# Performance work log

Hardware: AMD Instinct MI355X
Metric: run time of the kernel (lower is better)

The kernel has to match this reference:

```python
import jax, jax.numpy as jnp
import numpy as np

DIM = 32
N_HOP = 2
N_MEMORY = 32
BATCH = 2048
N_ENTITY = 100000
N_RELATION = 48


def _gru_cell(x, h, w_ih, w_hh, b_ih, b_hh):
    # PyTorch GRUCell semantics
    gi = x @ w_ih.T + b_ih          # [b, 3d]
    gh = h @ w_hh.T + b_hh          # [b, 3d]
    i_r, i_z, i_n = jnp.split(gi, 3, axis=-1)
    h_r, h_z, h_n = jnp.split(gh, 3, axis=-1)
    r = jax.nn.sigmoid(i_r + h_r)
    z = jax.nn.sigmoid(i_z + h_z)
    n = jnp.tanh(i_n + r * h_n)
    return (1.0 - z) * n + z * h


def setup_inputs() -> dict:
    key = jax.random.key(0)
    ks = jax.random.split(key, 16)
    h_i = jax.random.randint(ks[0], (BATCH, N_HOP, N_MEMORY), 0, N_ENTITY)
    R_i = jax.random.randint(ks[1], (BATCH, N_HOP, N_MEMORY), 0, N_RELATION)
    t_i = jax.random.randint(ks[2], (BATCH, N_HOP, N_MEMORY), 0, N_ENTITY)
    v_i = jax.random.randint(ks[3], (BATCH,), 0, N_ENTITY)
    s = 0.05
    entity_emb = jax.random.normal(ks[4], (N_ENTITY, DIM), jnp.float32) * s
    relation_emb = jax.random.normal(ks[5], (N_RELATION, DIM, DIM), jnp.float32) * s
    agg_w1 = jax.random.normal(ks[6], (DIM, 4 * DIM), jnp.float32) * s
    agg_b1 = jnp.zeros((DIM,), jnp.float32)
    agg_w2 = jax.random.normal(ks[7], (1, DIM), jnp.float32) * s
    agg_b2 = jnp.zeros((1,), jnp.float32)
    gru_w_ih = jax.random.normal(ks[8], (N_HOP, 3 * DIM, DIM), jnp.float32) * s
    gru_w_hh = jax.random.normal(ks[9], (N_HOP, 3 * DIM, DIM), jnp.float32) * s
    gru_b_ih = jnp.zeros((N_HOP, 3 * DIM), jnp.float32)
    gru_b_hh = jnp.zeros((N_HOP, 3 * DIM), jnp.float32)
    ans_w = jax.random.normal(ks[10], (DIM, DIM), jnp.float32) * s
    ans_b = jnp.zeros((DIM,), jnp.float32)
    return {
        'h_i': h_i, 'R_i': R_i, 't_i': t_i, 'v_i': v_i,
        'entity_emb': entity_emb, 'relation_emb': relation_emb,
        'agg_w1': agg_w1, 'agg_b1': agg_b1, 'agg_w2': agg_w2, 'agg_b2': agg_b2,
        'gru_w_ih': gru_w_ih, 'gru_w_hh': gru_w_hh,
        'gru_b_ih': gru_b_ih, 'gru_b_hh': gru_b_hh,
        'ans_w': ans_w, 'ans_b': ans_b,
    }


def reference(h_i, R_i, t_i, v_i, entity_emb, relation_emb,
              agg_w1, agg_b1, agg_w2, agg_b2,
              gru_w_ih, gru_w_hh, gru_b_ih, gru_b_hh,
              ans_w, ans_b):
    # InputModule: embedding gathers
    vs = entity_emb[v_i]                     # [b, d]
    hs = entity_emb[h_i]                     # [b, H, m, d]
    ts = entity_emb[t_i]                     # [b, H, m, d]
    Rs = relation_emb[R_i]                   # [b, H, m, d, d]

    M = vs
    n_hop = hs.shape[1]
    for hop in range(n_hop):
        R = Rs[:, hop]                       # [b, m, d, d]
        h = hs[:, hop]                       # [b, m, d]
        t = ts[:, hop]                       # [b, m, d]
        Rh = jnp.einsum('bmij,bmj->bmi', R, h)   # [b, m, d]
        vexp = vs[:, None, :]
        mexp = M[:, None, :]
        z = jnp.concatenate([Rh * vexp, Rh * mexp,
                             jnp.abs(Rh - vexp), jnp.abs(Rh - mexp)], axis=2)  # [b, m, 4d]
        # AggregateFnc: tanh(Linear) -> Linear(d,1); dropout is eval-mode identity
        Z = jnp.tanh(z @ agg_w1.T + agg_b1) @ agg_w2.T + agg_b2   # [b, m, 1]
        g = jax.nn.softmax(Z[..., 0], axis=1)[..., None]           # [b, m, 1]
        o = jnp.sum(t * g, axis=1)                                 # [b, d]
        M = _gru_cell(o, M, gru_w_ih[hop], gru_w_hh[hop],
                      gru_b_ih[hop], gru_b_hh[hop])
    # AnswerModule (dropout = identity in eval)
    Mw = jax.nn.sigmoid(M @ ans_w.T + ans_b)
    return jnp.sum(vs * Mw, axis=1)          # [b]
```

## Files before the change

kernel.cpp:

```cpp
#include <hip/hip_runtime.h>
#include <hip/hip_bf16.h>


#define NHOP 2

typedef __attribute__((ext_vector_type(4)))  float f32x4;
typedef __attribute__((ext_vector_type(8)))  short bf16x8s;
typedef __attribute__((ext_vector_type(4)))  int   i32x4;

__device__ __forceinline__ float sigmoid_f(float x){ return 1.0f/(1.0f+__expf(-x)); }
__device__ __forceinline__ float tanh_f(float x){
  float e = __expf(2.0f*x);
  return 1.0f - 2.0f/(e + 1.0f);
}
__device__ __forceinline__ unsigned pk_bf16(float lo, float hi){
  __hip_bfloat162 h = __float22bfloat162_rn(make_float2(lo, hi));
  return *reinterpret_cast<unsigned*>(&h);
}

__global__ __launch_bounds__(256) void ripple_fused(
    const int* __restrict__ h_i, const int* __restrict__ R_i, const int* __restrict__ t_i,
    const int* __restrict__ v_i,
    const float* __restrict__ entity_emb, const float* __restrict__ relation_emb,
    const float* __restrict__ agg_w1, const float* __restrict__ agg_b1,
    const float* __restrict__ agg_w2, const float* __restrict__ agg_b2,
    const float* __restrict__ gru_w_ih, const float* __restrict__ gru_w_hh,
    const float* __restrict__ gru_b_ih, const float* __restrict__ gru_b_hh,
    const float* __restrict__ ans_w, const float* __restrict__ ans_b,
    float* __restrict__ out)
{
  __shared__ __align__(16) int   s_bfrag[8*64*4];
  __shared__ __align__(16) float s_rhA[2][32*33];
  __shared__ __align__(16) float s_vsM[32*2];
  __shared__ __align__(16) float s_zpart[64];
  __shared__ __align__(16) float s_opart[8*32];
  __shared__ __align__(16) float s_M  [32];
  __shared__ __align__(16) float s_gig[192];

  const int b   = blockIdx.x;
  const int tid = threadIdx.x;
  const int g   = tid >> 5;
  const int o   = tid & 31;
  const int l   = tid & 63;
  const int w   = tid >> 6;
  const int c   = o & 7;
  const int r_  = o >> 3;
  const bool bb4 = (c & 4) != 0;
  const bool bb2 = (c & 2) != 0;
  const bool bb1 = (c & 1) != 0;

  #pragma unroll
  for (int k = 0; k < 2; ++k){
    int s  = tid + k*256;
    int f  = s >> 6, li = s & 63;
    int x  = f >> 1, ot = f & 1;
    const float* src = agg_w1 + (ot*16 + (li & 15))*128 + x*32 + ((li >> 4) & 3)*8;
    float4 f0 = *(const float4*)src;
    float4 f1 = *(const float4*)(src + 4);
    *(int4*)&s_bfrag[s*4] = make_int4((int)pk_bf16(f0.x, f0.y), (int)pk_bf16(f0.z, f0.w),
                                      (int)pk_bf16(f1.x, f1.y), (int)pk_bf16(f1.z, f1.w));
  }
  float Mreg = 0.f;
  if (tid < 32){
    float v = entity_emb[(size_t)v_i[b]*32 + o];
    s_vsM[o*2+0] = v; s_vsM[o*2+1] = v; s_M[o] = v;
    Mreg = v;
  }

  {
    const int iA = c*4 + r_;
    #pragma unroll 1
    for (int it = 0; it < 2*4; ++it){
      const int hp = it >> 2;
      const int ml = it & 3;
      const int ibase = (b*NHOP + hp)*32;
      int m    = g*4 + ml;
      int ridx = R_i[ibase + m];
      int hidx = h_i[ibase + m];
      const float* Rbase = relation_emb + (size_t)ridx*1024;
      float4 hv = *(const float4*)(entity_emb + (size_t)hidx*32 + c*4);
      float p[8];
      #pragma unroll
      for (int q = 0; q < 8; ++q){
        float4 rv = *(const float4*)(Rbase + q*128 + o*4);
        p[q] = rv.x*hv.x + rv.y*hv.y + rv.z*hv.z + rv.w*hv.w;
      }
      #pragma unroll
      for (int k = 0; k < 4; ++k){
        float send = bb4 ? p[k] : p[k+4];
        float t = __shfl_xor(send, 4);
        p[k] = (bb4 ? p[k+4] : p[k]) + t;
      }
      #pragma unroll
      for (int k = 0; k < 2; ++k){
        float send = bb2 ? p[k] : p[k+2];
        float t = __shfl_xor(send, 2);
        p[k] = (bb2 ? p[k+2] : p[k]) + t;
      }
      {
        float send = bb1 ? p[0] : p[1];
        float t = __shfl_xor(send, 1);
        p[0] = (bb1 ? p[1] : p[0]) + t;
      }
      s_rhA[hp][m*33 + iA] = p[0];
    }
  }
  __syncthreads();

  const int mt  = w >> 1, ot = w & 1;
  const int col = l & 15;
  const int kg  = l >> 4;
  const float b1o = agg_b1[ot*16 + col];
  const float w2o = agg_w2[ot*16 + col];

  for (int hop = 0; hop < NHOP; ++hop){
    const int ibase = (b*NHOP + hop)*32;

    float tv[4];
    #pragma unroll
    for (int ml = 0; ml < 4; ++ml)
      tv[ml] = entity_emb[(size_t)t_i[ibase + g*4 + ml]*32 + o];

    {
      const int m = mt*16 + col;
      const float* rp = &s_rhA[hop][m*33 + kg*8];
      float4 q0 = *(const float4*)(rp);
      float4 q1 = *(const float4*)(rp + 4);
      float rh[8] = {q0.x,q0.y,q0.z,q0.w,q1.x,q1.y,q1.z,q1.w};
      unsigned aw[4][4];
      #pragma unroll
      for (int q = 0; q < 4; ++q){
        int i0 = kg*8 + 2*q;
        float2 vm0 = *(const float2*)&s_vsM[i0*2];
        float2 vm1 = *(const float2*)&s_vsM[(i0+1)*2];
        float e0 = rh[2*q], e1 = rh[2*q+1];
        aw[0][q] = pk_bf16(e0*vm0.x,        e1*vm1.x);
        aw[1][q] = pk_bf16(e0*vm0.y,        e1*vm1.y);
        aw[2][q] = pk_bf16(fabsf(e0-vm0.x), fabsf(e1-vm1.x));
        aw[3][q] = pk_bf16(fabsf(e0-vm0.y), fabsf(e1-vm1.y));
      }
      f32x4 acc = {0.f, 0.f, 0.f, 0.f};
      #pragma unroll
      for (int x = 0; x < 4; ++x){
        i32x4 av = {(int)aw[x][0], (int)aw[x][1], (int)aw[x][2], (int)aw[x][3]};
        i32x4 bv = *(const i32x4*)&s_bfrag[((x*2 + ot)*64 + l)*4];
        acc = __builtin_amdgcn_mfma_f32_16x16x32_bf16(
                __builtin_bit_cast(bf16x8s, av),
                __builtin_bit_cast(bf16x8s, bv), acc, 0, 0, 0);
      }
      float v[4];
      #pragma unroll
      for (int r = 0; r < 4; ++r) v[r] = tanh_f(acc[r] + b1o) * w2o;
      const bool b3 = (l & 8) != 0;
      #pragma unroll
      for (int k = 0; k < 2; ++k){
        float send = b3 ? v[k] : v[k+2];
        float tt = __shfl_xor(send, 8);
        v[k] = (b3 ? v[k+2] : v[k]) + tt;
      }
      const bool b2_ = (l & 4) != 0;
      {
        float send = b2_ ? v[0] : v[1];
        float tt = __shfl_xor(send, 4);
        v[0] = (b2_ ? v[1] : v[0]) + tt;
      }
      v[0] += __shfl_xor(v[0], 2);
      v[0] += __shfl_xor(v[0], 1);
      if ((l & 3) == 0){
        int m_local = kg*4 + ((l >> 3) & 1)*2 + ((l >> 2) & 1);
        s_zpart[ot*32 + mt*16 + m_local] = v[0];
      }
    }
    __syncthreads();

    {
      float z  = s_zpart[o] + s_zpart[32 + o];
      float mx = z;
      #pragma unroll
      for (int s = 16; s > 0; s >>= 1) mx = fmaxf(mx, __shfl_xor(mx, s));
      float e  = __expf(z - mx);
      float sm = e;
      #pragma unroll
      for (int s = 16; s > 0; s >>= 1) sm += __shfl_xor(sm, s);
      float gval = e / sm;
      float po = 0.f;
      #pragma unroll
      for (int ml = 0; ml < 4; ++ml)
        po += __shfl(gval, g*4 + ml) * tv[ml];
      s_opart[g*32 + o] = po;
    }
    __syncthreads();

    {
      const int cc = (tid & 7) * 4;
      const int rr = tid >> 3;
      float4 o4 = make_float4(0,0,0,0);
      #pragma unroll
      for (int gg = 0; gg < 8; ++gg){
        float4 t = *(const float4*)&s_opart[gg*32 + cc];
        o4.x += t.x; o4.y += t.y; o4.z += t.z; o4.w += t.w;
      }
      float4 m4 = *(const float4*)&s_M[cc];
      #pragma unroll
      for (int k = 0; k < 3; ++k){
        int row = k*32 + rr;
        float4 wi = *(const float4*)(gru_w_ih + ((size_t)hop*96 + row)*32 + cc);
        float4 wh = *(const float4*)(gru_w_hh + ((size_t)hop*96 + row)*32 + cc);
        float ai = wi.x*o4.x + wi.y*o4.y + wi.z*o4.z + wi.w*o4.w;
        float ah = wh.x*m4.x + wh.y*m4.y + wh.z*m4.z + wh.w*m4.w;
        ai += __shfl_xor(ai,1); ai += __shfl_xor(ai,2); ai += __shfl_xor(ai,4);
        ah += __shfl_xor(ah,1); ah += __shfl_xor(ah,2); ah += __shfl_xor(ah,4);
        if ((tid & 7) == 0){
          s_gig[row]      = ai;
          s_gig[96 + row] = ah;
        }
      }
    }
    __syncthreads();

    if (tid < 32){
      const float* bih = gru_b_ih + hop*96;
      const float* bhh = gru_b_hh + hop*96;
      float ir = s_gig[o]       + bih[o];
      float iz = s_gig[32 + o]  + bih[32 + o];
      float in_= s_gig[64 + o]  + bih[64 + o];
      float hr = s_gig[96 + o]  + bhh[o];
      float hz = s_gig[128 + o] + bhh[32 + o];
      float hn = s_gig[160 + o] + bhh[64 + o];
      float r  = sigmoid_f(ir + hr);
      float zz = sigmoid_f(iz + hz);
      float n  = tanh_f(in_ + r*hn);
      float Mn = (1.f - zz)*n + zz*Mreg;
      Mreg = Mn;
      s_M[o] = Mn;
      s_vsM[o*2+1] = Mn;
    }
    __syncthreads();
  }

  {
    const int cc = (tid & 7) * 4;
    const int rr = tid >> 3;
    float4 m4 = *(const float4*)&s_M[cc];
    float4 aw = *(const float4*)(ans_w + (size_t)rr*32 + cc);
    float a = aw.x*m4.x + aw.y*m4.y + aw.z*m4.z + aw.w*m4.w;
    a += __shfl_xor(a,1); a += __shfl_xor(a,2); a += __shfl_xor(a,4);
    if ((tid & 7) == 0) s_zpart[rr] = sigmoid_f(a + ans_b[rr]);
  }
  __syncthreads();
  if (tid < 32){
    float val = s_vsM[o*2+0] * s_zpart[o];
    #pragma unroll
    for (int s = 16; s > 0; s >>= 1) val += __shfl_xor(val, s);
    if (tid == 0) out[b] = val;
  }
}

extern "C" void kernel_launch(void* const* d_in, const int* in_sizes, int n_in,
                              void* d_out, int out_size, void* d_ws, size_t ws_size,
                              hipStream_t stream) {
  const int*   h_i          = (const int*)  d_in[0];
  const int*   R_i          = (const int*)  d_in[1];
  const int*   t_i          = (const int*)  d_in[2];
  const int*   v_i          = (const int*)  d_in[3];
  const float* entity_emb   = (const float*)d_in[4];
  const float* relation_emb = (const float*)d_in[5];
  const float* agg_w1       = (const float*)d_in[6];
  const float* agg_b1       = (const float*)d_in[7];
  const float* agg_w2       = (const float*)d_in[8];
  const float* agg_b2       = (const float*)d_in[9];
  const float* gru_w_ih     = (const float*)d_in[10];
  const float* gru_w_hh     = (const float*)d_in[11];
  const float* gru_b_ih     = (const float*)d_in[12];
  const float* gru_b_hh     = (const float*)d_in[13];
  const float* ans_w        = (const float*)d_in[14];
  const float* ans_b        = (const float*)d_in[15];
  (void)agg_b2;
  float* outp = (float*)d_out;

  const int batch = in_sizes[3];
  ripple_fused<<<batch, 256, 0, stream>>>(
      h_i, R_i, t_i, v_i, entity_emb, relation_emb,
      agg_w1, agg_b1, agg_w2, agg_b2,
      gru_w_ih, gru_w_hh, gru_b_ih, gru_b_hh,
      ans_w, ans_b, outp);
}
```

Before: 45.28 us.

## Process two batch elements per block to amortize setup and weight loads

```diff
diff --git a/kernel.cpp b/kernel.cpp
--- a/kernel.cpp
+++ b/kernel.cpp
@@ -16,6 +16,23 @@
 __device__ __forceinline__ unsigned pk_bf16(float lo, float hi){
   __hip_bfloat162 h = __float22bfloat162_rn(make_float2(lo, hi));
   return *reinterpret_cast<unsigned*>(&h);
+}
+__device__ __forceinline__ float bfly8(float p[8], bool bb4, bool bb2, bool bb1){
+  #pragma unroll
+  for (int k = 0; k < 4; ++k){
+    float send = bb4 ? p[k] : p[k+4];
+    float t = __shfl_xor(send, 4);
+    p[k] = (bb4 ? p[k+4] : p[k]) + t;
+  }
+  #pragma unroll
+  for (int k = 0; k < 2; ++k){
+    float send = bb2 ? p[k] : p[k+2];
+    float t = __shfl_xor(send, 2);
+    p[k] = (bb2 ? p[k+2] : p[k]) + t;
+  }
+  float send = bb1 ? p[0] : p[1];
+  float t = __shfl_xor(send, 1);
+  return (bb1 ? p[1] : p[0]) + t;
 }
 
 __global__ __launch_bounds__(256) void ripple_fused(
@@ -27,17 +44,19 @@
     const float* __restrict__ gru_w_ih, const float* __restrict__ gru_w_hh,
     const float* __restrict__ gru_b_ih, const float* __restrict__ gru_b_hh,
     const float* __restrict__ ans_w, const float* __restrict__ ans_b,
-    float* __restrict__ out)
+    float* __restrict__ out, int batch)
 {
   __shared__ __align__(16) int   s_bfrag[8*64*4];
-  __shared__ __align__(16) float s_rhA[2][32*33];
-  __shared__ __align__(16) float s_vsM[32*2];
-  __shared__ __align__(16) float s_zpart[64];
-  __shared__ __align__(16) float s_opart[8*32];
-  __shared__ __align__(16) float s_M  [32];
-  __shared__ __align__(16) float s_gig[192];
-
-  const int b   = blockIdx.x;
+  __shared__ __align__(16) float s_rhA[2][2][32*33];
+  __shared__ __align__(16) float s_vsM[2][64];
+  __shared__ __align__(16) float s_zpart[2][64];
+  __shared__ __align__(16) float s_opart[2][4*32];
+  __shared__ __align__(16) float s_M[2][32];
+  __shared__ __align__(16) float s_gig[2][192];
+
+  const int bid = blockIdx.x;
+  const int eA  = bid*2;
+  const int eB  = (eA + 1 < batch) ? eA + 1 : eA;
   const int tid = threadIdx.x;
   const int g   = tid >> 5;
   const int o   = tid & 31;
@@ -53,56 +72,49 @@
   for (int k = 0; k < 2; ++k){
     int s  = tid + k*256;
     int f  = s >> 6, li = s & 63;
-    int x  = f >> 1, ot = f & 1;
-    const float* src = agg_w1 + (ot*16 + (li & 15))*128 + x*32 + ((li >> 4) & 3)*8;
+    int x  = f >> 1, otf = f & 1;
+    const float* src = agg_w1 + (otf*16 + (li & 15))*128 + x*32 + ((li >> 4) & 3)*8;
     float4 f0 = *(const float4*)src;
     float4 f1 = *(const float4*)(src + 4);
     *(int4*)&s_bfrag[s*4] = make_int4((int)pk_bf16(f0.x, f0.y), (int)pk_bf16(f0.z, f0.w),
                                       (int)pk_bf16(f1.x, f1.y), (int)pk_bf16(f1.z, f1.w));
   }
-  float Mreg = 0.f;
-  if (tid < 32){
-    float v = entity_emb[(size_t)v_i[b]*32 + o];
-    s_vsM[o*2+0] = v; s_vsM[o*2+1] = v; s_M[o] = v;
-    Mreg = v;
+  if (tid < 64){
+    int e  = tid >> 5, oo = tid & 31;
+    float v = entity_emb[(size_t)v_i[e ? eB : eA]*32 + oo];
+    s_vsM[e][oo*2+0] = v; s_vsM[e][oo*2+1] = v; s_M[e][oo] = v;
   }
 
   {
     const int iA = c*4 + r_;
     #pragma unroll 1
-    for (int it = 0; it < 2*4; ++it){
+    for (int it = 0; it < 8; ++it){
       const int hp = it >> 2;
       const int ml = it & 3;
-      const int ibase = (b*NHOP + hp)*32;
-      int m    = g*4 + ml;
-      int ridx = R_i[ibase + m];
-      int hidx = h_i[ibase + m];
-      const float* Rbase = relation_emb + (size_t)ridx*1024;
-      float4 hv = *(const float4*)(entity_emb + (size_t)hidx*32 + c*4);
-      float p[8];
+      const int m  = g*4 + ml;
+      int rAi = R_i[(eA*NHOP + hp)*32 + m];
+      int hAi = h_i[(eA*NHOP + hp)*32 + m];
+      int rBi = R_i[(eB*NHOP + hp)*32 + m];
+      int hBi = h_i[(eB*NHOP + hp)*32 + m];
+      const float* RbA = relation_emb + (size_t)rAi*1024;
+      const float* RbB = relation_emb + (size_t)rBi*1024;
+      float4 hvA = *(const float4*)(entity_emb + (size_t)hAi*32 + c*4);
+      float4 hvB = *(const float4*)(entity_emb + (size_t)hBi*32 + c*4);
+      float pA[8], pB[8];
       #pragma unroll
       for (int q = 0; q < 8; ++q){
-        float4 rv = *(const float4*)(Rbase + q*128 + o*4);
-        p[q] = rv.x*hv.x + rv.y*hv.y + rv.z*hv.z + rv.w*hv.w;
-      }
-      #pragma unroll
-      for (int k = 0; k < 4; ++k){
-        float send = bb4 ? p[k] : p[k+4];
-        float t = __shfl_xor(send, 4);
-        p[k] = (bb4 ? p[k+4] : p[k]) + t;
-      }
-      #pragma unroll
-      for (int k = 0; k < 2; ++k){
-        float send = bb2 ? p[k] : p[k+2];
-        float t = __shfl_xor(send, 2);
-        p[k] = (bb2 ? p[k+2] : p[k]) + t;
-      }
-      {
-        float send = bb1 ? p[0] : p[1];
-        float t = __shfl_xor(send, 1);
-        p[0] = (bb1 ? p[1] : p[0]) + t;
-      }
-      s_rhA[hp][m*33 + iA] = p[0];
+        float4 rv = *(const float4*)(RbA + q*128 + o*4);
+        pA[q] = rv.x*hvA.x + rv.y*hvA.y + rv.z*hvA.z + rv.w*hvA.w;
+      }
+      #pragma unroll
+      for (int q = 0; q < 8; ++q){
+        float4 rv = *(const float4*)(RbB + q*128 + o*4);
+        pB[q] = rv.x*hvB.x + rv.y*hvB.y + rv.z*hvB.z + rv.w*hvB.w;
+      }
+      float a0 = bfly8(pA, bb4, bb2, bb1);
+      float a1 = bfly8(pB, bb4, bb2, bb1);
+      s_rhA[0][hp][m*33 + iA] = a0;
+      s_rhA[1][hp][m*33 + iA] = a1;
     }
   }
   __syncthreads();
@@ -114,145 +126,163 @@
   const float w2o = agg_w2[ot*16 + col];
 
   for (int hop = 0; hop < NHOP; ++hop){
-    const int ibase = (b*NHOP + hop)*32;
-
-    float tv[4];
+    float tvA[4], tvB[4];
     #pragma unroll
-    for (int ml = 0; ml < 4; ++ml)
-      tv[ml] = entity_emb[(size_t)t_i[ibase + g*4 + ml]*32 + o];
+    for (int ml = 0; ml < 4; ++ml){
+      tvA[ml] = entity_emb[(size_t)t_i[(eA*NHOP + hop)*32 + g*4 + ml]*32 + o];
+      tvB[ml] = entity_emb[(size_t)t_i[(eB*NHOP + hop)*32 + g*4 + ml]*32 + o];
+    }
 
     {
-      const int m = mt*16 + col;
-      const float* rp = &s_rhA[hop][m*33 + kg*8];
-      float4 q0 = *(const float4*)(rp);
-      float4 q1 = *(const float4*)(rp + 4);
-      float rh[8] = {q0.x,q0.y,q0.z,q0.w,q1.x,q1.y,q1.z,q1.w};
-      unsigned aw[4][4];
-      #pragma unroll
-      for (int q = 0; q < 4; ++q){
-        int i0 = kg*8 + 2*q;
-        float2 vm0 = *(const float2*)&s_vsM[i0*2];
-        float2 vm1 = *(const float2*)&s_vsM[(i0+1)*2];
-        float e0 = rh[2*q], e1 = rh[2*q+1];
-        aw[0][q] = pk_bf16(e0*vm0.x,        e1*vm1.x);
-        aw[1][q] = pk_bf16(e0*vm0.y,        e1*vm1.y);
-        aw[2][q] = pk_bf16(fabsf(e0-vm0.x), fabsf(e1-vm1.x));
-        aw[3][q] = pk_bf16(fabsf(e0-vm0.y), fabsf(e1-vm1.y));
-      }
-      f32x4 acc = {0.f, 0.f, 0.f, 0.f};
-      #pragma unroll
-      for (int x = 0; x < 4; ++x){
-        i32x4 av = {(int)aw[x][0], (int)aw[x][1], (int)aw[x][2], (int)aw[x][3]};
-        i32x4 bv = *(const i32x4*)&s_bfrag[((x*2 + ot)*64 + l)*4];
-        acc = __builtin_amdgcn_mfma_f32_16x16x32_bf16(
-                __builtin_bit_cast(bf16x8s, av),
-                __builtin_bit_cast(bf16x8s, bv), acc, 0, 0, 0);
-      }
-      float v[4];
-      #pragma unroll
-      for (int r = 0; r < 4; ++r) v[r] = tanh_f(acc[r] + b1o) * w2o;
-      const bool b3 = (l & 8) != 0;
-      #pragma unroll
-      for (int k = 0; k < 2; ++k){
-        float send = b3 ? v[k] : v[k+2];
-        float tt = __shfl_xor(send, 8);
-        v[k] = (b3 ? v[k+2] : v[k]) + tt;
-      }
-      const bool b2_ = (l & 4) != 0;
-      {
-        float send = b2_ ? v[0] : v[1];
-        float tt = __shfl_xor(send, 4);
-        v[0] = (b2_ ? v[1] : v[0]) + tt;
-      }
-      v[0] += __shfl_xor(v[0], 2);
-      v[0] += __shfl_xor(v[0], 1);
-      if ((l & 3) == 0){
-        int m_local = kg*4 + ((l >> 3) & 1)*2 + ((l >> 2) & 1);
-        s_zpart[ot*32 + mt*16 + m_local] = v[0];
+      i32x4 bv[4];
+      #pragma unroll
+      for (int x = 0; x < 4; ++x)
+        bv[x] = *(const i32x4*)&s_bfrag[((x*2 + ot)*64 + l)*4];
+      #pragma unroll
+      for (int e = 0; e < 2; ++e){
+        const float* rp = &s_rhA[e][hop][(mt*16 + col)*33 + kg*8];
+        float4 q0 = *(const float4*)(rp);
+        float4 q1 = *(const float4*)(rp + 4);
+        float rh[8] = {q0.x,q0.y,q0.z,q0.w,q1.x,q1.y,q1.z,q1.w};
+        unsigned aw[4][4];
+        #pragma unroll
+        for (int q = 0; q < 4; ++q){
+          int i0 = kg*8 + 2*q;
+          float2 vm0 = *(const float2*)&s_vsM[e][i0*2];
+          float2 vm1 = *(const float2*)&s_vsM[e][(i0+1)*2];
+          float e0 = rh[2*q], e1 = rh[2*q+1];
+          aw[0][q] = pk_bf16(e0*vm0.x,        e1*vm1.x);
+          aw[1][q] = pk_bf16(e0*vm0.y,        e1*vm1.y);
+          aw[2][q] = pk_bf16(fabsf(e0-vm0.x), fabsf(e1-vm1.x));
+          aw[3][q] = pk_bf16(fabsf(e0-vm0.y), fabsf(e1-vm1.y));
+        }
+        f32x4 acc = {0.f, 0.f, 0.f, 0.f};
+        #pragma unroll
+        for (int x = 0; x < 4; ++x){
+          i32x4 av = {(int)aw[x][0], (int)aw[x][1], (int)aw[x][2], (int)aw[x][3]};
+          acc = __builtin_amdgcn_mfma_f32_16x16x32_bf16(
+                  __builtin_bit_cast(bf16x8s, av),
+                  __builtin_bit_cast(bf16x8s, bv[x]), acc, 0, 0, 0);
+        }
+        float v[4];
+        #pragma unroll
+        for (int r = 0; r < 4; ++r) v[r] = tanh_f(acc[r] + b1o) * w2o;
+        const bool b3 = (l & 8) != 0;
+        #pragma unroll
+        for (int k = 0; k < 2; ++k){
+          float send = b3 ? v[k] : v[k+2];
+          float tt = __shfl_xor(send, 8);
+          v[k] = (b3 ? v[k+2] : v[k]) + tt;
+        }
+        const bool b2_ = (l & 4) != 0;
+        {
+          float send = b2_ ? v[0] : v[1];
+          float tt = __shfl_xor(send, 4);
+          v[0] = (b2_ ? v[1] : v[0]) + tt;
+        }
+        v[0] += __shfl_xor(v[0], 2);
+        v[0] += __shfl_xor(v[0], 1);
+        if ((l & 3) == 0){
+          int m_local = kg*4 + ((l >> 3) & 1)*2 + ((l >> 2) & 1);
+          s_zpart[e][ot*32 + mt*16 + m_local] = v[0];
+        }
       }
     }
     __syncthreads();
 
-    {
-      float z  = s_zpart[o] + s_zpart[32 + o];
+    #pragma unroll
+    for (int e = 0; e < 2; ++e){
+      float z  = s_zpart[e][o] + s_zpart[e][32 + o];
       float mx = z;
       #pragma unroll
       for (int s = 16; s > 0; s >>= 1) mx = fmaxf(mx, __shfl_xor(mx, s));
-      float e  = __expf(z - mx);
-      float sm = e;
+      float ex = __expf(z - mx);
+      float sm = ex;
       #pragma unroll
       for (int s = 16; s > 0; s >>= 1) sm += __shfl_xor(sm, s);
-      float gval = e / sm;
+      float gval = ex / sm;
       float po = 0.f;
       #pragma unroll
       for (int ml = 0; ml < 4; ++ml)
-        po += __shfl(gval, g*4 + ml) * tv[ml];
-      s_opart[g*32 + o] = po;
+        po += __shfl(gval, g*4 + ml) * (e == 0 ? tvA[ml] : tvB[ml]);
+      po += __shfl_xor(po, 32);
+      if (l < 32) s_opart[e][w*32 + o] = po;
     }
     __syncthreads();
 
     {
       const int cc = (tid & 7) * 4;
       const int rr = tid >> 3;
-      float4 o4 = make_float4(0,0,0,0);
-      #pragma unroll
-      for (int gg = 0; gg < 8; ++gg){
-        float4 t = *(const float4*)&s_opart[gg*32 + cc];
-        o4.x += t.x; o4.y += t.y; o4.z += t.z; o4.w += t.w;
-      }
-      float4 m4 = *(const float4*)&s_M[cc];
+      float4 oA = make_float4(0,0,0,0), oB = make_float4(0,0,0,0);
+      #pragma unroll
+      for (int gg = 0; gg < 4; ++gg){
+        float4 ta = *(const float4*)&s_opart[0][gg*32 + cc];
+        float4 tb = *(const float4*)&s_opart[1][gg*32 + cc];
+        oA.x += ta.x; oA.y += ta.y; oA.z += ta.z; oA.w += ta.w;
+        oB.x += tb.x; oB.y += tb.y; oB.z += tb.z; oB.w += tb.w;
+      }
+      float4 mA = *(const float4*)&s_M[0][cc];
+      float4 mB = *(const float4*)&s_M[1][cc];
       #pragma unroll
       for (int k = 0; k < 3; ++k){
         int row = k*32 + rr;
         float4 wi = *(const float4*)(gru_w_ih + ((size_t)hop*96 + row)*32 + cc);
         float4 wh = *(const float4*)(gru_w_hh + ((size_t)hop*96 + row)*32 + cc);
-        float ai = wi.x*o4.x + wi.y*o4.y + wi.z*o4.z + wi.w*o4.w;
-        float ah = wh.x*m4.x + wh.y*m4.y + wh.z*m4.z + wh.w*m4.w;
-        ai += __shfl_xor(ai,1); ai += __shfl_xor(ai,2); ai += __shfl_xor(ai,4);
-        ah += __shfl_xor(ah,1); ah += __shfl_xor(ah,2); ah += __shfl_xor(ah,4);
+        float aiA = wi.x*oA.x + wi.y*oA.y + wi.z*oA.z + wi.w*oA.w;
+        float ahA = wh.x*mA.x + wh.y*mA.y + wh.z*mA.z + wh.w*mA.w;
+        float aiB = wi.x*oB.x + wi.y*oB.y + wi.z*oB.z + wi.w*oB.w;
+        float ahB = wh.x*mB.x + wh.y*mB.y + wh.z*mB.z + wh.w*mB.w;
+        aiA += __shfl_xor(aiA,1); aiA += __shfl_xor(aiA,2); aiA += __shfl_xor(aiA,4);
+        ahA += __shfl_xor(ahA,1); ahA += __shfl_xor(ahA,2); ahA += __shfl_xor(ahA,4);
+        aiB += __shfl_xor(aiB,1); aiB += __shfl_xor(aiB,2); aiB += __shfl_xor(aiB,4);
+        ahB += __shfl_xor(ahB,1); ahB += __shfl_xor(ahB,2); ahB += __shfl_xor(ahB,4);
         if ((tid & 7) == 0){
-          s_gig[row]      = ai;
-          s_gig[96 + row] = ah;
+          s_gig[0][row]      = aiA;
+          s_gig[0][96 + row] = ahA;
+          s_gig[1][row]      = aiB;
+          s_gig[1][96 + row] = ahB;
         }
       }
     }
     __syncthreads();
 
-    if (tid < 32){
+    if (tid < 64){
+      int e = tid >> 5, oo = tid & 31;
       const float* bih = gru_b_ih + hop*96;
       const float* bhh = gru_b_hh + hop*96;
-      float ir = s_gig[o]       + bih[o];
-      float iz = s_gig[32 + o]  + bih[32 + o];
-      float in_= s_gig[64 + o]  + bih[64 + o];
-      float hr = s_gig[96 + o]  + bhh[o];
-      float hz = s_gig[128 + o] + bhh[32 + o];
-      float hn = s_gig[160 + o] + bhh[64 + o];
+      float ir = s_gig[e][oo]       + bih[oo];
+      float iz = s_gig[e][32 + oo]  + bih[32 + oo];
+      float in_= s_gig[e][64 + oo]  + bih[64 + oo];
+      float hr = s_gig[e][96 + oo]  + bhh[oo];
+      float hz = s_gig[e][128 + oo] + bhh[32 + oo];
+      float hn = s_gig[e][160 + oo] + bhh[64 + oo];
       float r  = sigmoid_f(ir + hr);
       float zz = sigmoid_f(iz + hz);
       float n  = tanh_f(in_ + r*hn);
-      float Mn = (1.f - zz)*n + zz*Mreg;
-      Mreg = Mn;
-      s_M[o] = Mn;
-      s_vsM[o*2+1] = Mn;
+      float Mn = (1.f - zz)*n + zz*s_M[e][oo];
+      s_M[e][oo] = Mn;
+      s_vsM[e][oo*2+1] = Mn;
     }
     __syncthreads();
   }
 
-  {
+  #pragma unroll
+  for (int e = 0; e < 2; ++e){
     const int cc = (tid & 7) * 4;
     const int rr = tid >> 3;
-    float4 m4 = *(const float4*)&s_M[cc];
+    float4 m4 = *(const float4*)&s_M[e][cc];
     float4 aw = *(const float4*)(ans_w + (size_t)rr*32 + cc);
     float a = aw.x*m4.x + aw.y*m4.y + aw.z*m4.z + aw.w*m4.w;
     a += __shfl_xor(a,1); a += __shfl_xor(a,2); a += __shfl_xor(a,4);
-    if ((tid & 7) == 0) s_zpart[rr] = sigmoid_f(a + ans_b[rr]);
+    if ((tid & 7) == 0) s_zpart[e][rr] = sigmoid_f(a + ans_b[rr]);
   }
   __syncthreads();
-  if (tid < 32){
-    float val = s_vsM[o*2+0] * s_zpart[o];
+  if (tid < 64){
+    int e = tid >> 5, oo = tid & 31;
+    float val = s_vsM[e][oo*2+0] * s_zpart[e][oo];
     #pragma unroll
     for (int s = 16; s > 0; s >>= 1) val += __shfl_xor(val, s);
-    if (tid == 0) out[b] = val;
+    if (oo == 0) out[e ? eB : eA] = val;
   }
 }
 
@@ -279,9 +309,10 @@
   float* outp = (float*)d_out;
 
   const int batch = in_sizes[3];
-  ripple_fused<<<batch, 256, 0, stream>>>(
+  const int grid  = (batch + 1) / 2;
+  ripple_fused<<<grid, 256, 0, stream>>>(
       h_i, R_i, t_i, v_i, entity_emb, relation_emb,
       agg_w1, agg_b1, agg_w2, agg_b2,
       gru_w_ih, gru_w_hh, gru_b_ih, gru_b_hh,
-      ans_w, ans_b, outp);
-}
+      ans_w, ans_b, outp, batch);
+}
```

Result: faster. 42.21 us (-6.8%).
